# Performance work log

Hardware: AMD Instinct MI355X
Metric: run time of the kernel (lower is better)

The kernel has to match this reference:

```python
import jax, jax.numpy as jnp
import numpy as np

HEADS = 8
EPS = 1e-5
CONV_DIMS = [(16, 32), (32, 64), (64, 128), (128, 256), (256, 128), (128, 128)]


def _bn(x, g, b):
    # BatchNorm over the node dimension (training-mode batch statistics)
    m = x.mean(0)
    v = x.var(0)
    return (x - m) * jax.lax.rsqrt(v + EPS) * g + b


def _feast(x, src, dst, W, U, c, bias, n):
    # FeaStConv: q_h = softmax_h(u_h.(x_j - x_i) + c_h); out_i = mean_j sum_h q_h * (W_h x_j) + bias
    q = jax.nn.softmax((x[src] - x[dst]) @ U + c, axis=-1)          # [E, H]
    f = (x[src] @ W).reshape(src.shape[0], HEADS, -1)               # [E, H, C_out]
    msg = jnp.einsum('ehc,eh->ec', f, q)                            # [E, C_out]
    agg = jax.ops.segment_sum(msg, dst, num_segments=n)
    cnt = jax.ops.segment_sum(jnp.ones_like(dst, dtype=msg.dtype), dst, num_segments=n)
    return agg / cnt[:, None] + bias


def reference(pos, x, g0, b0, lin0_W, lin0_b,
              W0, U0, C0, B0, gc0, bc0,
              W1, U1, C1, B1, gc1, bc1,
              W2, U2, C2, B2, gc2, bc2,
              W3, U3, C3, B3, gc3, bc3,
              W4, U4, C4, B4, gc4, bc4,
              W5, U5, C5, B5, gc5, bc5,
              lin1_W, lin1_b, lin2_W, lin2_b, edge_index):
    n = pos.shape[0]
    loops = jnp.arange(n, dtype=edge_index.dtype)                   # PyG FeaStConv adds self-loops
    src = jnp.concatenate([edge_index[0], loops])
    dst = jnp.concatenate([edge_index[1], loops])

    h = _bn(pos, g0, b0)
    h = jnp.concatenate([h, x], axis=1)
    h = jax.nn.relu(h @ lin0_W + lin0_b)

    convs = [(W0, U0, C0, B0, gc0, bc0), (W1, U1, C1, B1, gc1, bc1),
             (W2, U2, C2, B2, gc2, bc2), (W3, U3, C3, B3, gc3, bc3),
             (W4, U4, C4, B4, gc4, bc4), (W5, U5, C5, B5, gc5, bc5)]
    for W, U, c, bias, g, b in convs:
        h = _feast(h, src, dst, W, U, c, bias, n)
        h = jax.nn.relu(_bn(h, g, b))

    h = jax.nn.relu(h @ lin1_W + lin1_b)
    return h @ lin2_W + lin2_b


def setup_inputs() -> dict:
    key = jax.random.key(0)
    N, E = 10000, 160000
    ks = iter(jax.random.split(key, 64))
    d = {}
    d['pos'] = jax.random.normal(next(ks), (N, 2), jnp.float32)
    d['x'] = jax.random.normal(next(ks), (N, 2), jnp.float32)
    d['edge_index'] = jax.random.randint(next(ks), (2, E), 0, N, dtype=jnp.int32)

    def lin(k, i, o):
        return jax.random.normal(k, (i, o), jnp.float32) * np.float32(1.0 / np.sqrt(i))

    d['g0'] = jnp.ones(2, jnp.float32); d['b0'] = jnp.zeros(2, jnp.float32)
    d['lin0_W'] = lin(next(ks), 4, 16); d['lin0_b'] = jnp.zeros(16, jnp.float32)
    for i, (ci, co) in enumerate(CONV_DIMS):
        d[f'W{i}'] = lin(next(ks), ci, HEADS * co)
        d[f'U{i}'] = lin(next(ks), ci, HEADS)
        d[f'C{i}'] = jnp.zeros(HEADS, jnp.float32)
        d[f'B{i}'] = jnp.zeros(co, jnp.float32)
        d[f'gc{i}'] = jnp.ones(co, jnp.float32)
        d[f'bc{i}'] = jnp.zeros(co, jnp.float32)
    d['lin1_W'] = lin(next(ks), 128, 64); d['lin1_b'] = jnp.zeros(64, jnp.float32)
    d['lin2_W'] = lin(next(ks), 64, 2); d['lin2_b'] = jnp.zeros(2, jnp.float32)
    return d
```

## Files before the change

### kernel.cpp

```cpp
#include <hip/hip_runtime.h>
#include <hip/hip_bf16.h>
#include <math.h>

#define HEADS 8
#define EPS 1e-5f

typedef __attribute__((ext_vector_type(8))) _Float16 half8;
typedef __attribute__((ext_vector_type(4))) _Float16 half4;
typedef __attribute__((ext_vector_type(2))) _Float16 half2v;
typedef __attribute__((ext_vector_type(4))) float f32x4;

__device__ __forceinline__ unsigned short f2h(float f) {
    union { _Float16 h; unsigned short u; } v;
    v.h = (_Float16)f;
    return v.u;
}

#define PACK_TOTAL 745472
#define PACK_BLOCKS 2912

__global__ void k_setup1(const float* __restrict__ W0, const float* __restrict__ W1,
                         const float* __restrict__ W2, const float* __restrict__ W3,
                         const float* __restrict__ W4, const float* __restrict__ W5,
                         unsigned short* __restrict__ Bp,
                         const int* __restrict__ ei, int* __restrict__ deg,
                         const float* __restrict__ pos, float* __restrict__ pstats,
                         int E, int N, int degBlocks) {
    int b = blockIdx.x, tid = threadIdx.x;
    if (b < PACK_BLOCKS) {
        int idx = b * 256 + tid;
        const int CI[6]  = {16, 32, 64, 128, 256, 128};
        const int CO[6]  = {32, 64, 128, 256, 128, 128};
        const int COP[6] = {64, 64, 128, 256, 128, 128};
        const int OFF[7] = {0, 8192, 24576, 90112, 352256, 614400, 745472};
        int L = 0;
        while (idx >= OFF[L + 1]) ++L;
        const float* W = L == 0 ? W0 : L == 1 ? W1 : L == 2 ? W2 : L == 3 ? W3 : L == 4 ? W4 : W5;
        int rel = idx - OFF[L];
        int j = rel & 7;
        int lane = (rel >> 3) & 63;
        int t = rel >> 9;
        int nT = COP[L] >> 4;
        int nt = t % nT, kt = t / nT;
        int kk = kt * 32 + ((lane >> 4) << 3) + j;
        int c  = (nt << 4) + (lane & 15);
        int ci = CI[L], co = CO[L];
        float v = 0.f;
        if (c < co) {
            int h = kk / ci, ko = kk % ci;
            v = W[ko * (HEADS * co) + h * co + c];
        }
        Bp[idx] = f2h(v);
    } else if (b < PACK_BLOCKS + degBlocks) {
        int e = (b - PACK_BLOCKS) * 256 + tid;
        int E2 = E + N;
        if (e < E2) {
            int dst = (e < E) ? ei[E + e] : (e - E);
            atomicAdd(&deg[dst], 1);
        }
    } else {
        int gid = (b - PACK_BLOCKS - degBlocks) * 256 + tid;
        int stride = 64 * 256;
        float s0 = 0, s1 = 0, q0 = 0, q1 = 0;
        for (int i = gid; i < N; i += stride) {
            float a = pos[i * 2], bb = pos[i * 2 + 1];
            s0 += a; s1 += bb; q0 += a * a; q1 += bb * bb;
        }
        __shared__ float red[256][4];
        red[tid][0] = s0; red[tid][1] = s1; red[tid][2] = q0; red[tid][3] = q1;
        __syncthreads();
        for (int off = 128; off > 0; off >>= 1) {
            if (tid < off) {
                red[tid][0] += red[tid + off][0]; red[tid][1] += red[tid + off][1];
                red[tid][2] += red[tid + off][2]; red[tid][3] += red[tid + off][3];
            }
            __syncthreads();
        }
        if (tid == 0) {
            atomicAdd(&pstats[0], red[0][0]); atomicAdd(&pstats[1], red[0][1]);
            atomicAdd(&pstats[2], red[0][2]); atomicAdd(&pstats[3], red[0][3]);
        }
    }
}

__global__ void k_scan(const int* __restrict__ deg, int* __restrict__ row_ptr, int n) {
    __shared__ int part[1024];
    int t = threadIdx.x;
    int chunk = (n + 1023) >> 10;
    int begin = t * chunk;
    int end = begin + chunk;
    if (begin > n) begin = n;
    if (end > n) end = n;
    int s = 0;
    for (int i = begin; i < end; ++i) s += deg[i];
    part[t] = s;
    __syncthreads();
    for (int off = 1; off < 1024; off <<= 1) {
        int v = (t >= off) ? part[t - off] : 0;
        __syncthreads();
        part[t] += v;
        __syncthreads();
    }
    int run = (t == 0) ? 0 : part[t - 1];
    for (int i = begin; i < end; ++i) { row_ptr[i] = run; run += deg[i]; }
    if (t == 1023) row_ptr[n] = part[1023];
}

__global__ void k_setup2(const int* __restrict__ ei, const int* __restrict__ row_ptr,
                         int* __restrict__ fill, int* __restrict__ src_sorted,
                         const float* __restrict__ pos, const float* __restrict__ x,
                         const float* __restrict__ pstats, const float* __restrict__ g0,
                         const float* __restrict__ b0, const float* __restrict__ W,
                         const float* __restrict__ bias, const float* __restrict__ U0,
                         _Float16* __restrict__ out, float* __restrict__ xu0,
                         int E, int N, int fillBlocks) {
    int b = blockIdx.x, tid = threadIdx.x;
    if (b < fillBlocks) {
        int e = b * 256 + tid;
        int E2 = E + N;
        if (e < E2) {
            int srcv, dst;
            if (e < E) { srcv = ei[e]; dst = ei[E + e]; } else { srcv = e - E; dst = srcv; }
            int p = atomicAdd(&fill[dst], 1);
            src_sorted[row_ptr[dst] + p] = srcv;
        }
    } else {
        int i = (b - fillBlocks) * 256 + tid;
        if (i >= N) return;
        float invn = 1.0f / (float)N;
        float in4[4];
        #pragma unroll
        for (int j = 0; j < 2; ++j) {
            float m = pstats[j] * invn;
            float v = pstats[2 + j] * invn - m * m;
            in4[j] = (pos[i * 2 + j] - m) * rsqrtf(v + EPS) * g0[j] + b0[j];
        }
        in4[2] = x[i * 2]; in4[3] = x[i * 2 + 1];
        float o16[16];
        #pragma unroll
        for (int o = 0; o < 16; ++o) {
            float s = bias[o];
            #pragma unroll
            for (int j = 0; j < 4; ++j) s += in4[j] * W[j * 16 + o];
            o16[o] = fmaxf(s, 0.f);
            out[i * 16 + o] = (_Float16)o16[o];
        }
        #pragma unroll
        for (int hh = 0; hh < 8; ++hh) {
            float p = 0.f;
            #pragma unroll
            for (int k = 0; k < 16; ++k) p += o16[k] * U0[k * 8 + hh];
            xu0[i * 8 + hh] = p;
        }
    }
}

__device__ __forceinline__ void chunk_softmax(const float* __restrict__ xu,
        const int* __restrict__ srcs, int base, int cnt, int lane,
        float4 xi0, float4 xi1, float4 c0, float4 c1, float dinv,
        float* __restrict__ qrow, int* __restrict__ srow) {
    if (lane < cnt) {
        int s = srcs[base + lane];
        float4 xs0 = *(const float4*)(xu + (size_t)s * 8);
        float4 xs1 = *(const float4*)(xu + (size_t)s * 8 + 4);
        float t[8];
        t[0] = xs0.x - xi0.x + c0.x; t[1] = xs0.y - xi0.y + c0.y;
        t[2] = xs0.z - xi0.z + c0.z; t[3] = xs0.w - xi0.w + c0.w;
        t[4] = xs1.x - xi1.x + c1.x; t[5] = xs1.y - xi1.y + c1.y;
        t[6] = xs1.z - xi1.z + c1.z; t[7] = xs1.w - xi1.w + c1.w;
        float mx = t[0];
        #pragma unroll
        for (int h = 1; h < 8; ++h) mx = fmaxf(mx, t[h]);
        float sum = 0.f;
        #pragma unroll
        for (int h = 0; h < 8; ++h) { t[h] = __expf(t[h] - mx); sum += t[h]; }
        float qs = dinv / sum;
        float4 q0 = {t[0] * qs, t[1] * qs, t[2] * qs, t[3] * qs};
        float4 q1 = {t[4] * qs, t[5] * qs, t[6] * qs, t[7] * qs};
        *(float4*)(qrow + lane * 8) = q0;
        *(float4*)(qrow + lane * 8 + 4) = q1;
        srow[lane] = s;
    }
}

template<int V>
__global__ __launch_bounds__(256) void k_gather_big(const _Float16* __restrict__ hin,
        const float* __restrict__ xu, const float* __restrict__ chead,
        const int* __restrict__ row_ptr, const int* __restrict__ srcs,
        unsigned short* __restrict__ S, int n, int ci) {
    __shared__ float qbuf[4][64 * 8];
    __shared__ int   sbuf[4][64];
    int w = threadIdx.x >> 6, lane = threadIdx.x & 63;
    int i = blockIdx.x * 4 + w;
    if (i >= n) return;
    int rp0 = row_ptr[i], rp1 = row_ptr[i + 1];
    float dinv = 1.f / (float)(rp1 - rp0);
    float4 xi0 = *(const float4*)(xu + (size_t)i * 8);
    float4 xi1 = *(const float4*)(xu + (size_t)i * 8 + 4);
    float4 c0 = *(const float4*)chead;
    float4 c1 = *(const float4*)(chead + 4);
    int kb = lane * V;
    float acc[8][V];
    #pragma unroll
    for (int hh = 0; hh < 8; ++hh)
        #pragma unroll
        for (int v = 0; v < V; ++v) acc[hh][v] = 0.f;

    for (int base = rp0; base < rp1; base += 64) {
        int cnt = rp1 - base; if (cnt > 64) cnt = 64;
        chunk_softmax(xu, srcs, base, cnt, lane, xi0, xi1, c0, c1, dinv, qbuf[w], sbuf[w]);
        int j = 0;
        for (; j + 1 < cnt; j += 2) {
            int s0 = sbuf[w][j], s1 = sbuf[w][j + 1];
            const _Float16* h0 = hin + (size_t)s0 * ci + kb;
            const _Float16* h1 = hin + (size_t)s1 * ci + kb;
            float xv0[V], xv1[V];
            if (V == 4) {
                half4 f0 = *(const half4*)h0, f1 = *(const half4*)h1;
                #pragma unroll
                for (int v = 0; v < 4; ++v) { xv0[v] = (float)f0[v]; xv1[v] = (float)f1[v]; }
            } else if (V == 2) {
                half2v f0 = *(const half2v*)h0, f1 = *(const half2v*)h1;
                #pragma unroll
                for (int v = 0; v < 2; ++v) { xv0[v] = (float)f0[v]; xv1[v] = (float)f1[v]; }
            } else { xv0[0] = (float)h0[0]; xv1[0] = (float)h1[0]; }
            const float4* qa = (const float4*)(qbuf[w] + j * 8);
            const float4* qc = (const float4*)(qbuf[w] + (j + 1) * 8);
            float4 qa0 = qa[0], qa1 = qa[1], qb0 = qc[0], qb1 = qc[1];
            float qA[8] = {qa0.x, qa0.y, qa0.z, qa0.w, qa1.x, qa1.y, qa1.z, qa1.w};
            float qB[8] = {qb0.x, qb0.y, qb0.z, qb0.w, qb1.x, qb1.y, qb1.z, qb1.w};
            #pragma unroll
            for (int hh = 0; hh < 8; ++hh)
                #pragma unroll
                for (int v = 0; v < V; ++v)
                    acc[hh][v] += qA[hh] * xv0[v] + qB[hh] * xv1[v];
        }
        if (j < cnt) {
            int s0 = sbuf[w][j];
            const _Float16* h0 = hin + (size_t)s0 * ci + kb;
            float xv0[V];
            if (V == 4) {
                half4 f = *(const half4*)h0;
                for (int v = 0; v < 4; ++v) xv0[v] = (float)f[v];
            } else if (V == 2) {
                half2v f = *(const half2v*)h0;
                for (int v = 0; v < 2; ++v) xv0[v] = (float)f[v];
            } else {
                xv0[0] = (float)h0[0];
            }
            const float4* qa = (const float4*)(qbuf[w] + j * 8);
            float4 qa0 = qa[0], qa1 = qa[1];
            float qA[8] = {qa0.x, qa0.y, qa0.z, qa0.w, qa1.x, qa1.y, qa1.z, qa1.w};
            #pragma unroll
            for (int hh = 0; hh < 8; ++hh)
                #pragma unroll
                for (int v = 0; v < V; ++v) acc[hh][v] += qA[hh] * xv0[v];
        }
    }
    #pragma unroll
    for (int hh = 0; hh < 8; ++hh) {
        unsigned short o[V];
        #pragma unroll
        for (int v = 0; v < V; ++v) o[v] = f2h(acc[hh][v]);
        unsigned short* sp = S + (size_t)i * 8 * ci + hh * ci + kb;
        if (V == 4)      *(ushort4*)sp = *(ushort4*)o;
        else if (V == 2) *(ushort2*)sp = *(ushort2*)o;
        else             sp[0] = o[0];
    }
}

template<int V2>
__global__ __launch_bounds__(256) void k_gather_small(const _Float16* __restrict__ hin,
        const float* __restrict__ xu, const float* __restrict__ chead,
        const int* __restrict__ row_ptr, const int* __restrict__ srcs,
        unsigned short* __restrict__ S, int n) {
    const int ci = 8 * V2;
    __shared__ float qbuf[4][64 * 8];
    __shared__ int   sbuf[4][64];
    int w = threadIdx.x >> 6, lane = threadIdx.x & 63;
    int i = blockIdx.x * 4 + w;
    if (i >= n) return;
    int rp0 = row_ptr[i], rp1 = row_ptr[i + 1];
    float dinv = 1.f / (float)(rp1 - rp0);
    float4 xi0 = *(const float4*)(xu + (size_t)i * 8);
    float4 xi1 = *(const float4*)(xu + (size_t)i * 8 + 4);
    float4 c0 = *(const float4*)chead;
    float4 c1 = *(const float4*)(chead + 4);
    int hh = lane >> 3;
    int kb = (lane & 7) * V2;
    float acc[V2];
    #pragma unroll
    for (int v = 0; v < V2; ++v) acc[v] = 0.f;

    for (int base = rp0; base < rp1; base += 64) {
        int cnt = rp1 - base; if (cnt > 64) cnt = 64;
        chunk_softmax(xu, srcs, base, cnt, lane, xi0, xi1, c0, c1, dinv, qbuf[w], sbuf[w]);
        int j = 0;
        for (; j + 1 < cnt; j += 2) {
            int s0 = sbuf[w][j], s1 = sbuf[w][j + 1];
            const _Float16* h0 = hin + (size_t)s0 * ci + kb;
            const _Float16* h1 = hin + (size_t)s1 * ci + kb;
            float xv0[V2], xv1[V2];
            if (V2 == 4) {
                half4 f0 = *(const half4*)h0, f1 = *(const half4*)h1;
                #pragma unroll
                for (int v = 0; v < 4; ++v) { xv0[v] = (float)f0[v]; xv1[v] = (float)f1[v]; }
            } else {
                half2v f0 = *(const half2v*)h0, f1 = *(const half2v*)h1;
                #pragma unroll
                for (int v = 0; v < 2; ++v) { xv0[v] = (float)f0[v]; xv1[v] = (float)f1[v]; }
            }
            float q0 = qbuf[w][j * 8 + hh];
            float q1 = qbuf[w][(j + 1) * 8 + hh];
            #pragma unroll
            for (int v = 0; v < V2; ++v) acc[v] += q0 * xv0[v] + q1 * xv1[v];
        }
        if (j < cnt) {
            int s0 = sbuf[w][j];
            const _Float16* h0 = hin + (size_t)s0 * ci + kb;
            float xv0[V2];
            if (V2 == 4) {
                half4 f = *(const half4*)h0;
                for (int v = 0; v < 4; ++v) xv0[v] = (float)f[v];
            } else {
                half2v f = *(const half2v*)h0;
                for (int v = 0; v < 2; ++v) xv0[v] = (float)f[v];
            }
            float q0 = qbuf[w][j * 8 + hh];
            #pragma unroll
            for (int v = 0; v < V2; ++v) acc[v] += q0 * xv0[v];
        }
    }
    unsigned short o[V2];
    #pragma unroll
    for (int v = 0; v < V2; ++v) o[v] = f2h(acc[v]);
    unsigned short* sp = S + (size_t)i * 8 * ci + hh * ci + kb;
    if (V2 == 4) *(ushort4*)sp = *(ushort4*)o;
    else         *(ushort2*)sp = *(ushort2*)o;
}

__global__ __launch_bounds__(256) void k_gemm_stats(const unsigned short* __restrict__ A,
        const unsigned short* __restrict__ Bp, float* __restrict__ z,
        float* __restrict__ stats, int M, int K, int co, int nTtot) {
    int tid = threadIdx.x;
    int w = tid >> 6, lane = tid & 63;
    int quad = lane >> 4, l16 = lane & 15;
    int m0 = blockIdx.x * 64;
    int n0 = blockIdx.y * 64;
    int nt0 = n0 >> 4;
    int m = m0 + w * 16 + l16;
    int mc = m < M ? m : M - 1;
    const half8* Ap = (const half8*)(A + (size_t)mc * K) + quad;
    const half8* Bb = (const half8*)Bp;
    f32x4 acc[4] = {};
    int nsteps = K >> 5;
    for (int ks = 0; ks < nsteps; ++ks) {
        half8 a = Ap[ks * 4];
        long bbase = ((long)ks * nTtot + nt0) * 64 + lane;
        #pragma unroll
        for (int ct = 0; ct < 4; ++ct) {
            half8 b = Bb[bbase + ct * 64];
            acc[ct] = __builtin_amdgcn_mfma_f32_16x16x32_f16(a, b, acc[ct], 0, 0, 0);
        }
    }
    __shared__ float sred[64][4];
    __shared__ float qred[64][4];
    #pragma unroll
    for (int ct = 0; ct < 4; ++ct) {
        int colb = ct * 16 + l16;
        int col = n0 + colb;
        float s = 0.f, q = 0.f;
        #pragma unroll
        for (int r = 0; r < 4; ++r) {
            int row = m0 + w * 16 + quad * 4 + r;
            bool ok = row < M;
            float v = ok ? acc[ct][r] : 0.f;
            if (ok && col < co) z[(size_t)row * co + col] = v;
            s += v; q += v * v;
        }
        s += __shfl_xor(s, 16, 64); q += __shfl_xor(q, 16, 64);
        s += __shfl_xor(s, 32, 64); q += __shfl_xor(q, 32, 64);
        if (quad == 0) { sred[colb][w] = s; qred[colb][w] = q; }
    }
    __syncthreads();
    if (tid < 64 && (n0 + tid) < co) {
        float s = sred[tid][0] + sred[tid][1] + sred[tid][2] + sred[tid][3];
        float q = qred[tid][0] + qred[tid][1] + qred[tid][2] + qred[tid][3];
        atomicAdd(&stats[n0 + tid], s);
        atomicAdd(&stats[co + n0 + tid], q);
    }
}

template<int V>
__global__ __launch_bounds__(256) void k_bnx(const float* __restrict__ z,
        const float* __restrict__ stats, const float* __restrict__ g,
        const float* __restrict__ b, const float* __restrict__ Un,
        _Float16* __restrict__ hout, float* __restrict__ xun, int n, int co) {
    int w = threadIdx.x >> 6, lane = threadIdx.x & 63;
    int node = blockIdx.x * 4 + w;
    if (node >= n) return;
    int c0 = lane * V;
    bool act = c0 < co;
    float invn = 1.f / (float)n;
    float hv[V];
    #pragma unroll
    for (int v = 0; v < V; ++v) hv[v] = 0.f;
    if (act) {
        const float* zp = z + (size_t)node * co + c0;
        float zv[V];
        if (V == 4) { float4 f = *(const float4*)zp; zv[0] = f.x; zv[1] = f.y; zv[2] = f.z; zv[3] = f.w; }
        else if (V == 2) { float2 f = *(const float2*)zp; zv[0] = f.x; zv[1] = f.y; }
        else zv[0] = zp[0];
        #pragma unroll
        for (int v = 0; v < V; ++v) {
            int cch = c0 + v;
            float mm = stats[cch] * invn;
            float vr = stats[co + cch] * invn - mm * mm;
            hv[v] = fmaxf((zv[v] - mm) * rsqrtf(vr + EPS) * g[cch] + b[cch], 0.f);
        }
        _Float16* hp = hout + (size_t)node * co + c0;
        if (V == 4) { half4 f = {(_Float16)hv[0], (_Float16)hv[1], (_Float16)hv[2], (_Float16)hv[3]}; *(half4*)hp = f; }
        else if (V == 2) { half2v f = {(_Float16)hv[0], (_Float16)hv[1]}; *(half2v*)hp = f; }
        else hp[0] = (_Float16)hv[0];
    }
    if (Un) {
        float p[8];
        #pragma unroll
        for (int hh = 0; hh < 8; ++hh) p[hh] = 0.f;
        if (act) {
            #pragma unroll
            for (int v = 0; v < V; ++v)
                #pragma unroll
                for (int hh = 0; hh < 8; ++hh) p[hh] += hv[v] * Un[(c0 + v) * 8 + hh];
        }
        #pragma unroll
        for (int hh = 0; hh < 8; ++hh) {
            #pragma unroll
            for (int off = 32; off; off >>= 1) p[hh] += __shfl_xor(p[hh], off, 64);
        }
        float mine = 0.f;
        #pragma unroll
        for (int hh = 0; hh < 8; ++hh) if (lane == hh) mine = p[hh];
        if (lane < 8) xun[node * 8 + lane] = mine;
    }
}

__global__ __launch_bounds__(256) void k_bnlin(const float* __restrict__ z,
        const float* __restrict__ stats, const float* __restrict__ g,
        const float* __restrict__ b, const float* __restrict__ W1,
        const float* __restrict__ b1, const float* __restrict__ W2,
        const float* __restrict__ b2, float* __restrict__ out, int n) {
    __shared__ float hbuf[4][128];
    int w = threadIdx.x >> 6, lane = threadIdx.x & 63;
    int node = blockIdx.x * 4 + w;
    if (node >= n) return;
    float invn = 1.f / (float)n;
    float2 zv = *(const float2*)(z + (size_t)node * 128 + lane * 2);
    float zr[2] = {zv.x, zv.y};
    #pragma unroll
    for (int v = 0; v < 2; ++v) {
        int c = lane * 2 + v;
        float mm = stats[c] * invn;
        float vr = stats[128 + c] * invn - mm * mm;
        hbuf[w][c] = fmaxf((zr[v] - mm) * rsqrtf(vr + EPS) * g[c] + b[c], 0.f);
    }
    float s = b1[lane];
    #pragma unroll 8
    for (int k = 0; k < 128; ++k) s += hbuf[w][k] * W1[k * 64 + lane];
    float r = fmaxf(s, 0.f);
    float p0 = r * W2[lane * 2];
    float p1 = r * W2[lane * 2 + 1];
    #pragma unroll
    for (int off = 32; off > 0; off >>= 1) {
        p0 += __shfl_down(p0, off, 64);
        p1 += __shfl_down(p1, off, 64);
    }
    if (lane == 0) {
        out[node * 2] = p0 + b2[0];
        out[node * 2 + 1] = p1 + b2[1];
    }
}

extern "C" void kernel_launch(void* const* d_in, const int* in_sizes, int n_in,
                              void* d_out, int out_size, void* d_ws, size_t ws_size,
                              hipStream_t stream) {
    const float* pos    = (const float*)d_in[0];
    const float* x      = (const float*)d_in[1];
    const int*   ei     = (const int*)d_in[2];
    const float* g0     = (const float*)d_in[3];
    const float* b0     = (const float*)d_in[4];
    const float* lin0_W = (const float*)d_in[5];
    const float* lin0_b = (const float*)d_in[6];
    const float* lin1_W = (const float*)d_in[43];
    const float* lin1_b = (const float*)d_in[44];
    const float* lin2_W = (const float*)d_in[45];
    const float* lin2_b = (const float*)d_in[46];

    int N = in_sizes[0] / 2;
    int E = in_sizes[2] / 2;
    int E2 = E + N;

    static const int CI[6]  = {16, 32, 64, 128, 256, 128};
    static const int CO[6]  = {32, 64, 128, 256, 128, 128};
    static const int COP[6] = {64, 64, 128, 256, 128, 128};
    static const int BPOFF[6] = {0, 8192, 24576, 90112, 352256, 614400};

    char* p = (char*)d_ws;
    auto alloc = [&](size_t bytes) -> char* {
        char* r = p;
        p += (bytes + 255) & ~(size_t)255;
        return r;
    };
    unsigned short* BpAll = (unsigned short*)alloc((size_t)PACK_TOTAL * 2);
    char* zr = alloc(((size_t)2 * N + 4 + 6 * 512) * 4);
    int*   deg      = (int*)zr;
    int*   fill     = deg + N;
    float* pstats   = (float*)(fill + N);
    float* statsAll = pstats + 4;
    size_t zr_bytes = ((size_t)2 * N + 4 + 6 * 512) * 4;

    int* row_ptr    = (int*)alloc(((size_t)N + 1) * 4);
    int* src_sorted = (int*)alloc((size_t)E2 * 4);
    float* xu       = (float*)alloc((size_t)N * 8 * 4);
    unsigned short* S = (unsigned short*)alloc((size_t)N * 2048 * 2);
    float* z        = (float*)alloc((size_t)N * 256 * 4);
    _Float16* hA    = (_Float16*)alloc((size_t)N * 256 * 2);
    _Float16* hB    = (_Float16*)alloc((size_t)N * 256 * 2);

    hipMemsetAsync(zr, 0, zr_bytes, stream);

    const int tpb = 256;
    int degBlocks = (E2 + tpb - 1) / tpb;
    int fillBlocks = degBlocks;
    int frontBlocks = (N + tpb - 1) / tpb;

    k_setup1<<<PACK_BLOCKS + degBlocks + 64, tpb, 0, stream>>>(
        (const float*)d_in[7], (const float*)d_in[13], (const float*)d_in[19],
        (const float*)d_in[25], (const float*)d_in[31], (const float*)d_in[37], BpAll,
        ei, deg, pos, pstats, E, N, degBlocks);
    k_scan<<<1, 1024, 0, stream>>>(deg, row_ptr, N);
    k_setup2<<<fillBlocks + frontBlocks, tpb, 0, stream>>>(
        ei, row_ptr, fill, src_sorted, pos, x, pstats, g0, b0, lin0_W, lin0_b,
        (const float*)d_in[8], hA, xu, E, N, fillBlocks);

    _Float16* hin = hA;
    _Float16* hout = hB;
    for (int L = 0; L < 6; ++L) {
        int ci = CI[L], co = CO[L], coP = COP[L];
        const float* Ch = (const float*)d_in[7 + L * 6 + 2];
        const float* gc = (const float*)d_in[7 + L * 6 + 4];
        const float* bc = (const float*)d_in[7 + L * 6 + 5];
        const float* Un = (L < 5) ? (const float*)d_in[7 + (L + 1) * 6 + 1] : nullptr;
        int K = HEADS * ci;
        float* statsL = statsAll + L * 512;

        int ggrid = (N + 3) / 4;
        if (ci == 16)       k_gather_small<2><<<ggrid, 256, 0, stream>>>(hin, xu, Ch, row_ptr, src_sorted, S, N);
        else if (ci == 32)  k_gather_small<4><<<ggrid, 256, 0, stream>>>(hin, xu, Ch, row_ptr, src_sorted, S, N);
        else if (ci == 64)  k_gather_big<1><<<ggrid, 256, 0, stream>>>(hin, xu, Ch, row_ptr, src_sorted, S, N, ci);
        else if (ci == 128) k_gather_big<2><<<ggrid, 256, 0, stream>>>(hin, xu, Ch, row_ptr, src_sorted, S, N, ci);
        else                k_gather_big<4><<<ggrid, 256, 0, stream>>>(hin, xu, Ch, row_ptr, src_sorted, S, N, ci);

        dim3 g((N + 63) / 64, coP / 64);
        k_gemm_stats<<<g, 256, 0, stream>>>(S, BpAll + BPOFF[L], z, statsL, N, K, co, coP / 16);

        int bgrid = (N + 3) / 4;
        if (L < 5) {
            if (co >= 256)      k_bnx<4><<<bgrid, 256, 0, stream>>>(z, statsL, gc, bc, Un, hout, xu, N, co);
            else if (co >= 128) k_bnx<2><<<bgrid, 256, 0, stream>>>(z, statsL, gc, bc, Un, hout, xu, N, co);
            else                k_bnx<1><<<bgrid, 256, 0, stream>>>(z, statsL, gc, bc, Un, hout, xu, N, co);
            _Float16* t = hin; hin = hout; hout = t;
        } else {
            k_bnlin<<<bgrid, 256, 0, stream>>>(z, statsL, gc, bc, lin1_W, lin1_b, lin2_W, lin2_b,
                                               (float*)d_out, N);
        }
    }
}
```

Measured before the change: 449.3 us.

## Fuse BatchNorm+ReLU into gather and store pre-norm activations in fp16

The GEMM now writes the pre-BatchNorm output z as fp16 instead of fp32. The next layer's gather kernels apply the previous layer's BN affine and ReLU on the fly while loading neighbor features, so the per-layer k_bnx kernel no longer writes an h buffer. It becomes k_xu, which only computes the xu projection. This halves z traffic and removes one full activation write and read per layer, at the cost of recomputing BN+ReLU once per edge instead of once per node. The gather loops also drop their 2-way unroll, and fp16 storage of pre-norm values carries a slight precision risk.

```diff
diff --git a/kernel.cpp b/kernel.cpp
--- a/kernel.cpp
+++ b/kernel.cpp
@@ -184,7 +184,9 @@
 }
 
 template<int V>
-__global__ __launch_bounds__(256) void k_gather_big(const _Float16* __restrict__ hin,
+__global__ __launch_bounds__(256) void k_gather_big(const _Float16* __restrict__ zin,
+        const float* __restrict__ stats, const float* __restrict__ g,
+        const float* __restrict__ b,
         const float* __restrict__ xu, const float* __restrict__ chead,
         const int* __restrict__ row_ptr, const int* __restrict__ srcs,
         unsigned short* __restrict__ S, int n, int ci) {
@@ -200,6 +202,21 @@
     float4 c0 = *(const float4*)chead;
     float4 c1 = *(const float4*)(chead + 4);
     int kb = lane * V;
+    float sc[V], bo[V];
+    if (stats) {
+        float invn = 1.f / (float)n;
+        #pragma unroll
+        for (int v = 0; v < V; ++v) {
+            int c = kb + v;
+            float m = stats[c] * invn;
+            float var = stats[ci + c] * invn - m * m;
+            float s = g[c] * rsqrtf(var + EPS);
+            sc[v] = s; bo[v] = b[c] - m * s;
+        }
+    } else {
+        #pragma unroll
+        for (int v = 0; v < V; ++v) { sc[v] = 1.f; bo[v] = 0.f; }
+    }
     float acc[8][V];
     #pragma unroll
     for (int hh = 0; hh < 8; ++hh)
@@ -209,44 +226,20 @@
     for (int base = rp0; base < rp1; base += 64) {
         int cnt = rp1 - base; if (cnt > 64) cnt = 64;
         chunk_softmax(xu, srcs, base, cnt, lane, xi0, xi1, c0, c1, dinv, qbuf[w], sbuf[w]);
-        int j = 0;
-        for (; j + 1 < cnt; j += 2) {
-            int s0 = sbuf[w][j], s1 = sbuf[w][j + 1];
-            const _Float16* h0 = hin + (size_t)s0 * ci + kb;
-            const _Float16* h1 = hin + (size_t)s1 * ci + kb;
-            float xv0[V], xv1[V];
-            if (V == 4) {
-                half4 f0 = *(const half4*)h0, f1 = *(const half4*)h1;
-                #pragma unroll
-                for (int v = 0; v < 4; ++v) { xv0[v] = (float)f0[v]; xv1[v] = (float)f1[v]; }
-            } else if (V == 2) {
-                half2v f0 = *(const half2v*)h0, f1 = *(const half2v*)h1;
-                #pragma unroll
-                for (int v = 0; v < 2; ++v) { xv0[v] = (float)f0[v]; xv1[v] = (float)f1[v]; }
-            } else { xv0[0] = (float)h0[0]; xv1[0] = (float)h1[0]; }
-            const float4* qa = (const float4*)(qbuf[w] + j * 8);
-            const float4* qc = (const float4*)(qbuf[w] + (j + 1) * 8);
-            float4 qa0 = qa[0], qa1 = qa[1], qb0 = qc[0], qb1 = qc[1];
-            float qA[8] = {qa0.x, qa0.y, qa0.z, qa0.w, qa1.x, qa1.y, qa1.z, qa1.w};
-            float qB[8] = {qb0.x, qb0.y, qb0.z, qb0.w, qb1.x, qb1.y, qb1.z, qb1.w};
-            #pragma unroll
-            for (int hh = 0; hh < 8; ++hh)
-                #pragma unroll
-                for (int v = 0; v < V; ++v)
-                    acc[hh][v] += qA[hh] * xv0[v] + qB[hh] * xv1[v];
-        }
-        if (j < cnt) {
-            int s0 = sbuf[w][j];
-            const _Float16* h0 = hin + (size_t)s0 * ci + kb;
-            float xv0[V];
+        for (int j = 0; j < cnt; ++j) {
+            int s = sbuf[w][j];
+            const _Float16* h0 = zin + (size_t)s * ci + kb;
+            float xv[V];
             if (V == 4) {
                 half4 f = *(const half4*)h0;
-                for (int v = 0; v < 4; ++v) xv0[v] = (float)f[v];
+                #pragma unroll
+                for (int v = 0; v < 4; ++v) xv[v] = fmaxf((float)f[v] * sc[v] + bo[v], 0.f);
             } else if (V == 2) {
                 half2v f = *(const half2v*)h0;
-                for (int v = 0; v < 2; ++v) xv0[v] = (float)f[v];
+                #pragma unroll
+                for (int v = 0; v < 2; ++v) xv[v] = fmaxf((float)f[v] * sc[v] + bo[v], 0.f);
             } else {
-                xv0[0] = (float)h0[0];
+                xv[0] = fmaxf((float)h0[0] * sc[0] + bo[0], 0.f);
             }
             const float4* qa = (const float4*)(qbuf[w] + j * 8);
             float4 qa0 = qa[0], qa1 = qa[1];
@@ -254,7 +247,7 @@
             #pragma unroll
             for (int hh = 0; hh < 8; ++hh)
                 #pragma unroll
-                for (int v = 0; v < V; ++v) acc[hh][v] += qA[hh] * xv0[v];
+                for (int v = 0; v < V; ++v) acc[hh][v] += qA[hh] * xv[v];
         }
     }
     #pragma unroll
@@ -270,7 +263,9 @@
 }
 
 template<int V2>
-__global__ __launch_bounds__(256) void k_gather_small(const _Float16* __restrict__ hin,
+__global__ __launch_bounds__(256) void k_gather_small(const _Float16* __restrict__ zin,
+        const float* __restrict__ stats, const float* __restrict__ g,
+        const float* __restrict__ b,
         const float* __restrict__ xu, const float* __restrict__ chead,
         const int* __restrict__ row_ptr, const int* __restrict__ srcs,
         unsigned short* __restrict__ S, int n) {
@@ -288,6 +283,21 @@
     float4 c1 = *(const float4*)(chead + 4);
     int hh = lane >> 3;
     int kb = (lane & 7) * V2;
+    float sc[V2], bo[V2];
+    if (stats) {
+        float invn = 1.f / (float)n;
+        #pragma unroll
+        for (int v = 0; v < V2; ++v) {
+            int c = kb + v;
+            float m = stats[c] * invn;
+            float var = stats[ci + c] * invn - m * m;
+            float s = g[c] * rsqrtf(var + EPS);
+            sc[v] = s; bo[v] = b[c] - m * s;
+        }
+    } else {
+        #pragma unroll
+        for (int v = 0; v < V2; ++v) { sc[v] = 1.f; bo[v] = 0.f; }
+    }
     float acc[V2];
     #pragma unroll
     for (int v = 0; v < V2; ++v) acc[v] = 0.f;
@@ -295,40 +305,22 @@
     for (int base = rp0; base < rp1; base += 64) {
         int cnt = rp1 - base; if (cnt > 64) cnt = 64;
         chunk_softmax(xu, srcs, base, cnt, lane, xi0, xi1, c0, c1, dinv, qbuf[w], sbuf[w]);
-        int j = 0;
-        for (; j + 1 < cnt; j += 2) {
-            int s0 = sbuf[w][j], s1 = sbuf[w][j + 1];
-            const _Float16* h0 = hin + (size_t)s0 * ci + kb;
-            const _Float16* h1 = hin + (size_t)s1 * ci + kb;
-            float xv0[V2], xv1[V2];
-            if (V2 == 4) {
-                half4 f0 = *(const half4*)h0, f1 = *(const half4*)h1;
-                #pragma unroll
-                for (int v = 0; v < 4; ++v) { xv0[v] = (float)f0[v]; xv1[v] = (float)f1[v]; }
-            } else {
-                half2v f0 = *(const half2v*)h0, f1 = *(const half2v*)h1;
-                #pragma unroll
-                for (int v = 0; v < 2; ++v) { xv0[v] = (float)f0[v]; xv1[v] = (float)f1[v]; }
-            }
-            float q0 = qbuf[w][j * 8 + hh];
-            float q1 = qbuf[w][(j + 1) * 8 + hh];
-            #pragma unroll
-            for (int v = 0; v < V2; ++v) acc[v] += q0 * xv0[v] + q1 * xv1[v];
-        }
-        if (j < cnt) {
-            int s0 = sbuf[w][j];
-            const _Float16* h0 = hin + (size_t)s0 * ci + kb;
-            float xv0[V2];
+        for (int j = 0; j < cnt; ++j) {
+            int s = sbuf[w][j];
+            const _Float16* h0 = zin + (size_t)s * ci + kb;
+            float xv[V2];
             if (V2 == 4) {
                 half4 f = *(const half4*)h0;
-                for (int v = 0; v < 4; ++v) xv0[v] = (float)f[v];
+                #pragma unroll
+                for (int v = 0; v < 4; ++v) xv[v] = fmaxf((float)f[v] * sc[v] + bo[v], 0.f);
             } else {
                 half2v f = *(const half2v*)h0;
-                for (int v = 0; v < 2; ++v) xv0[v] = (float)f[v];
+                #pragma unroll
+                for (int v = 0; v < 2; ++v) xv[v] = fmaxf((float)f[v] * sc[v] + bo[v], 0.f);
             }
             float q0 = qbuf[w][j * 8 + hh];
             #pragma unroll
-            for (int v = 0; v < V2; ++v) acc[v] += q0 * xv0[v];
+            for (int v = 0; v < V2; ++v) acc[v] += q0 * xv[v];
         }
     }
     unsigned short o[V2];
@@ -340,7 +332,7 @@
 }
 
 __global__ __launch_bounds__(256) void k_gemm_stats(const unsigned short* __restrict__ A,
-        const unsigned short* __restrict__ Bp, float* __restrict__ z,
+        const unsigned short* __restrict__ Bp, _Float16* __restrict__ z,
         float* __restrict__ stats, int M, int K, int co, int nTtot) {
     int tid = threadIdx.x;
     int w = tid >> 6, lane = tid & 63;
@@ -375,7 +367,7 @@
             int row = m0 + w * 16 + quad * 4 + r;
             bool ok = row < M;
             float v = ok ? acc[ct][r] : 0.f;
-            if (ok && col < co) z[(size_t)row * co + col] = v;
+            if (ok && col < co) z[(size_t)row * co + col] = (_Float16)v;
             s += v; q += v * v;
         }
         s += __shfl_xor(s, 16, 64); q += __shfl_xor(q, 16, 64);
@@ -392,60 +384,47 @@
 }
 
 template<int V>
-__global__ __launch_bounds__(256) void k_bnx(const float* __restrict__ z,
+__global__ __launch_bounds__(256) void k_xu(const _Float16* __restrict__ z,
         const float* __restrict__ stats, const float* __restrict__ g,
         const float* __restrict__ b, const float* __restrict__ Un,
-        _Float16* __restrict__ hout, float* __restrict__ xun, int n, int co) {
+        float* __restrict__ xun, int n, int co) {
     int w = threadIdx.x >> 6, lane = threadIdx.x & 63;
     int node = blockIdx.x * 4 + w;
     if (node >= n) return;
     int c0 = lane * V;
     bool act = c0 < co;
     float invn = 1.f / (float)n;
-    float hv[V];
-    #pragma unroll
-    for (int v = 0; v < V; ++v) hv[v] = 0.f;
+    float p[8];
+    #pragma unroll
+    for (int hh = 0; hh < 8; ++hh) p[hh] = 0.f;
     if (act) {
-        const float* zp = z + (size_t)node * co + c0;
-        float zv[V];
-        if (V == 4) { float4 f = *(const float4*)zp; zv[0] = f.x; zv[1] = f.y; zv[2] = f.z; zv[3] = f.w; }
-        else if (V == 2) { float2 f = *(const float2*)zp; zv[0] = f.x; zv[1] = f.y; }
-        else zv[0] = zp[0];
+        const _Float16* zp = z + (size_t)node * co + c0;
+        float hv[V];
         #pragma unroll
         for (int v = 0; v < V; ++v) {
-            int cch = c0 + v;
-            float mm = stats[cch] * invn;
-            float vr = stats[co + cch] * invn - mm * mm;
-            hv[v] = fmaxf((zv[v] - mm) * rsqrtf(vr + EPS) * g[cch] + b[cch], 0.f);
-        }
-        _Float16* hp = hout + (size_t)node * co + c0;
-        if (V == 4) { half4 f = {(_Float16)hv[0], (_Float16)hv[1], (_Float16)hv[2], (_Float16)hv[3]}; *(half4*)hp = f; }
-        else if (V == 2) { half2v f = {(_Float16)hv[0], (_Float16)hv[1]}; *(half2v*)hp = f; }
-        else hp[0] = (_Float16)hv[0];
-    }
-    if (Un) {
-        float p[8];
-        #pragma unroll
-        for (int hh = 0; hh < 8; ++hh) p[hh] = 0.f;
-        if (act) {
+            int c = c0 + v;
+            float m = stats[c] * invn;
+            float var = stats[co + c] * invn - m * m;
+            float s = g[c] * rsqrtf(var + EPS);
+            hv[v] = fmaxf((float)zp[v] * s + (b[c] - m * s), 0.f);
+        }
+        #pragma unroll
+        for (int v = 0; v < V; ++v)
             #pragma unroll
-            for (int v = 0; v < V; ++v)
-                #pragma unroll
-                for (int hh = 0; hh < 8; ++hh) p[hh] += hv[v] * Un[(c0 + v) * 8 + hh];
-        }
-        #pragma unroll
-        for (int hh = 0; hh < 8; ++hh) {
-            #pragma unroll
-            for (int off = 32; off; off >>= 1) p[hh] += __shfl_xor(p[hh], off, 64);
-        }
-        float mine = 0.f;
-        #pragma unroll
-        for (int hh = 0; hh < 8; ++hh) if (lane == hh) mine = p[hh];
-        if (lane < 8) xun[node * 8 + lane] = mine;
-    }
-}
-
-__global__ __launch_bounds__(256) void k_bnlin(const float* __restrict__ z,
+            for (int hh = 0; hh < 8; ++hh) p[hh] += hv[v] * Un[(c0 + v) * 8 + hh];
+    }
+    #pragma unroll
+    for (int hh = 0; hh < 8; ++hh) {
+        #pragma unroll
+        for (int off = 32; off; off >>= 1) p[hh] += __shfl_xor(p[hh], off, 64);
+    }
+    float mine = 0.f;
+    #pragma unroll
+    for (int hh = 0; hh < 8; ++hh) if (lane == hh) mine = p[hh];
+    if (lane < 8) xun[node * 8 + lane] = mine;
+}
+
+__global__ __launch_bounds__(256) void k_bnlin(const _Float16* __restrict__ z,
         const float* __restrict__ stats, const float* __restrict__ g,
         const float* __restrict__ b, const float* __restrict__ W1,
         const float* __restrict__ b1, const float* __restrict__ W2,
@@ -455,14 +434,14 @@
     int node = blockIdx.x * 4 + w;
     if (node >= n) return;
     float invn = 1.f / (float)n;
-    float2 zv = *(const float2*)(z + (size_t)node * 128 + lane * 2);
-    float zr[2] = {zv.x, zv.y};
+    half2v zv = *(const half2v*)(z + (size_t)node * 128 + lane * 2);
     #pragma unroll
     for (int v = 0; v < 2; ++v) {
         int c = lane * 2 + v;
         float mm = stats[c] * invn;
         float vr = stats[128 + c] * invn - mm * mm;
-        hbuf[w][c] = fmaxf((zr[v] - mm) * rsqrtf(vr + EPS) * g[c] + b[c], 0.f);
+        float s = g[c] * rsqrtf(vr + EPS);
+        hbuf[w][c] = fmaxf((float)zv[v] * s + (b[c] - mm * s), 0.f);
     }
     float s = b1[lane];
     #pragma unroll 8
@@ -523,9 +502,8 @@
     int* src_sorted = (int*)alloc((size_t)E2 * 4);
     float* xu       = (float*)alloc((size_t)N * 8 * 4);
     unsigned short* S = (unsigned short*)alloc((size_t)N * 2048 * 2);
-    float* z        = (float*)alloc((size_t)N * 256 * 4);
-    _Float16* hA    = (_Float16*)alloc((size_t)N * 256 * 2);
-    _Float16* hB    = (_Float16*)alloc((size_t)N * 256 * 2);
+    _Float16* z     = (_Float16*)alloc((size_t)N * 256 * 2);
+    _Float16* hA    = (_Float16*)alloc((size_t)N * 16 * 2);
 
     hipMemsetAsync(zr, 0, zr_bytes, stream);
 
@@ -543,8 +521,6 @@
         ei, row_ptr, fill, src_sorted, pos, x, pstats, g0, b0, lin0_W, lin0_b,
         (const float*)d_in[8], hA, xu, E, N, fillBlocks);
 
-    _Float16* hin = hA;
-    _Float16* hout = hB;
     for (int L = 0; L < 6; ++L) {
         int ci = CI[L], co = CO[L], coP = COP[L];
         const float* Ch = (const float*)d_in[7 + L * 6 + 2];
@@ -554,22 +530,26 @@
         int K = HEADS * ci;
         float* statsL = statsAll + L * 512;
 
+        const _Float16* zin = (L == 0) ? hA : z;
+        const float* pstatsL = (L == 0) ? nullptr : statsAll + (L - 1) * 512;
+        const float* gPrev   = (L == 0) ? nullptr : (const float*)d_in[7 + (L - 1) * 6 + 4];
+        const float* bPrev   = (L == 0) ? nullptr : (const float*)d_in[7 + (L - 1) * 6 + 5];
+
         int ggrid = (N + 3) / 4;
-        if (ci == 16)       k_gather_small<2><<<ggrid, 256, 0, stream>>>(hin, xu, Ch, row_ptr, src_sorted, S, N);
-        else if (ci == 32)  k_gather_small<4><<<ggrid, 256, 0, stream>>>(hin, xu, Ch, row_ptr, src_sorted, S, N);
-        else if (ci == 64)  k_gather_big<1><<<ggrid, 256, 0, stream>>>(hin, xu, Ch, row_ptr, src_sorted, S, N, ci);
-        else if (ci == 128) k_gather_big<2><<<ggrid, 256, 0, stream>>>(hin, xu, Ch, row_ptr, src_sorted, S, N, ci);
-        else                k_gather_big<4><<<ggrid, 256, 0, stream>>>(hin, xu, Ch, row_ptr, src_sorted, S, N, ci);
+        if (ci == 16)       k_gather_small<2><<<ggrid, 256, 0, stream>>>(zin, pstatsL, gPrev, bPrev, xu, Ch, row_ptr, src_sorted, S, N);
+        else if (ci == 32)  k_gather_small<4><<<ggrid, 256, 0, stream>>>(zin, pstatsL, gPrev, bPrev, xu, Ch, row_ptr, src_sorted, S, N);
+        else if (ci == 64)  k_gather_big<1><<<ggrid, 256, 0, stream>>>(zin, pstatsL, gPrev, bPrev, xu, Ch, row_ptr, src_sorted, S, N, ci);
+        else if (ci == 128) k_gather_big<2><<<ggrid, 256, 0, stream>>>(zin, pstatsL, gPrev, bPrev, xu, Ch, row_ptr, src_sorted, S, N, ci);
+        else                k_gather_big<4><<<ggrid, 256, 0, stream>>>(zin, pstatsL, gPrev, bPrev, xu, Ch, row_ptr, src_sorted, S, N, ci);
 
         dim3 g((N + 63) / 64, coP / 64);
         k_gemm_stats<<<g, 256, 0, stream>>>(S, BpAll + BPOFF[L], z, statsL, N, K, co, coP / 16);
 
         int bgrid = (N + 3) / 4;
         if (L < 5) {
-            if (co >= 256)      k_bnx<4><<<bgrid, 256, 0, stream>>>(z, statsL, gc, bc, Un, hout, xu, N, co);
-            else if (co >= 128) k_bnx<2><<<bgrid, 256, 0, stream>>>(z, statsL, gc, bc, Un, hout, xu, N, co);
-            else                k_bnx<1><<<bgrid, 256, 0, stream>>>(z, statsL, gc, bc, Un, hout, xu, N, co);
-            _Float16* t = hin; hin = hout; hout = t;
+            if (co >= 256)      k_xu<4><<<bgrid, 256, 0, stream>>>(z, statsL, gc, bc, Un, xu, N, co);
+            else if (co >= 128) k_xu<2><<<bgrid, 256, 0, stream>>>(z, statsL, gc, bc, Un, xu, N, co);
+            else                k_xu<1><<<bgrid, 256, 0, stream>>>(z, statsL, gc, bc, Un, xu, N, co);
         } else {
             k_bnlin<<<bgrid, 256, 0, stream>>>(z, statsL, gc, bc, lin1_W, lin1_b, lin2_W, lin2_b,
                                                (float*)d_out, N);
```

Measured after the change: 441.9 us, median of 2. Within noise of the previous version (-1.6%).
